# Optimization experiments

Measured on AMD Instinct MI355X. Metric: run time of the kernel, lower is better.

The kernel has to match this reference:

```python
import jax, jax.numpy as jnp
import numpy as np
from jax import lax

B_, NCH, T = 128, 22, 1000
F1, F2 = 8, 16
BN_EPS = 1e-5


def _conv(x, w, b, pad, groups=1):
    y = lax.conv_general_dilated(x, w, (1, 1), pad,
                                 dimension_numbers=('NCHW', 'OIHW', 'NCHW'),
                                 feature_group_count=groups)
    return y if b is None else y + b[None, :, None, None]


def _bn(x, g, b):
    # eval-mode BatchNorm2d with running_mean=0, running_var=1
    return x * (g / np.sqrt(1.0 + BN_EPS))[None, :, None, None] + b[None, :, None, None]


def _avgpool(x, w, s):
    y = lax.reduce_window(x, 0.0, lax.add, (1, 1, 1, w), (1, 1, 1, s), 'VALID')
    return y / w


def _ln(x, g, b):
    m = x.mean(-1, keepdims=True)
    v = ((x - m) ** 2).mean(-1, keepdims=True)
    return (x - m) * lax.rsqrt(v + 1e-5) * g + b


def _enc_layer(h, qw, qb, pw, pb, f1w, f1b, f2w, f2b, g1, b1, g2, b2):
    # h: (S, N, E). Torch TransformerEncoderLayer default is seq-first, so axis 0
    # (the STDCNN batch dim) is attended over -- faithfully reproduced here.
    S, N, E = h.shape
    H = 8
    hd = E // H
    q, k, v = jnp.split(h @ qw.T + qb, 3, axis=-1)
    q = q.reshape(S, N, H, hd)
    k = k.reshape(S, N, H, hd)
    v = v.reshape(S, N, H, hd)
    att = jax.nn.softmax(jnp.einsum('snhd,tnhd->nhst', q, k) / np.sqrt(hd), axis=-1)
    o = jnp.einsum('nhst,tnhd->snhd', att, v).reshape(S, N, E) @ pw.T + pb
    h = _ln(h + o, g1, b1)
    ff = jax.nn.relu(h @ f1w.T + f1b) @ f2w.T + f2b
    return _ln(h + ff, g2, b2)


def setup_inputs() -> dict:
    key = jax.random.key(0)
    ks = iter(jax.random.split(key, 48))

    def nrm(shape, s=0.1):
        return jax.random.normal(next(ks), shape, jnp.float32) * s

    inp = dict(
        x=jax.random.normal(next(ks), (B_, 1, NCH, T), jnp.float32),
        w_spec1=nrm((F1, 1, 1, 125)), b_spec1=nrm((F1,)),
        w_spec2=nrm((F1, 1, 1, 30)), b_spec2=nrm((F1,)),
        g_bn1=1.0 + nrm((F1,)), b_bn1=nrm((F1,)),
        g_bn2=1.0 + nrm((F1,)), b_bn2=nrm((F1,)),
        w_sp1a=nrm((F2, 1, NCH, 1)),
        g_bn3=1.0 + nrm((F2,)), b_bn3=nrm((F2,)),
        w_sp1b=nrm((F2, F2, 1, 1)), b_sp1b=nrm((F2,)),
        g_bn4=1.0 + nrm((F2,)), b_bn4=nrm((F2,)),
        w_sp2=nrm((F2, F1, NCH, 1)), b_sp2=nrm((F2,)),
        g_bn5=1.0 + nrm((F2,)), b_bn5=nrm((F2,)),
        A=jnp.eye(F2, dtype=jnp.float32) + nrm((F2, F2), 0.01),
        Bm=nrm((F2, F2)),
        Cm=jnp.eye(F2, dtype=jnp.float32) + nrm((F2, F2), 0.01),
        qkv_w=nrm((2, 3 * F2, F2)), qkv_b=nrm((2, 3 * F2)),
        proj_w=nrm((2, F2, F2)), proj_b=nrm((2, F2)),
        ff1_w=nrm((2, 64, F2)), ff1_b=nrm((2, 64)),
        ff2_w=nrm((2, F2, 64)), ff2_b=nrm((2, F2)),
        ln1_g=jnp.ones((2, F2), jnp.float32), ln1_b=jnp.zeros((2, F2), jnp.float32),
        ln2_g=jnp.ones((2, F2), jnp.float32), ln2_b=jnp.zeros((2, F2), jnp.float32),
    )
    return inp


def reference(x, w_spec1, b_spec1, w_spec2, b_spec2, g_bn1, b_bn1, g_bn2, b_bn2,
              w_sp1a, g_bn3, b_bn3, w_sp1b, b_sp1b, g_bn4, b_bn4,
              w_sp2, b_sp2, g_bn5, b_bn5, A, Bm, Cm,
              qkv_w, qkv_b, proj_w, proj_b, ff1_w, ff1_b, ff2_w, ff2_b,
              ln1_g, ln1_b, ln2_g, ln2_b):
    # spectral branches (torch 'same' padding: k=125 -> (62,62); k=30 -> (14,15))
    x1 = _bn(_conv(x, w_spec1, b_spec1, [(0, 0), (62, 62)]), g_bn1, b_bn1)
    x2 = _bn(_conv(x, w_spec2, b_spec2, [(0, 0), (14, 15)]), g_bn2, b_bn2)
    # spatial branch 1 (dropout is identity in eval)
    s1 = jax.nn.elu(_bn(_conv(x1, w_sp1a, None, 'VALID', groups=F1), g_bn3, b_bn3))
    s1 = jax.nn.elu(_bn(_conv(s1, w_sp1b, b_sp1b, 'VALID'), g_bn4, b_bn4))
    s1 = _avgpool(s1, 32, 32)                                   # (B,16,1,31)
    # spatial branch 2: square -> avgpool -> log(clamp)
    s2 = _bn(_conv(x2, w_sp2, b_sp2, 'VALID'), g_bn5, b_bn5)
    s2 = jnp.log(jnp.clip(_avgpool(jnp.square(s2), 75, 25), 1e-6))  # (B,16,1,38)
    xc = jnp.concatenate([s1, s2], axis=3)                       # (B,16,1,69)
    Bn, Cc, H2, W2 = xc.shape
    seq = xc.reshape(Bn, Cc, H2 * W2).transpose(0, 2, 1)         # (B,L,16)

    # linear SSM recurrence (torch for-loop -> lax.scan)
    def step(state, xt):
        state = state @ A + xt @ Bm.T
        return state, state @ Cm.T

    _, outs = lax.scan(step, jnp.zeros((Bn, F2), seq.dtype), seq.transpose(1, 0, 2))
    h = outs.transpose(1, 0, 2)                                  # (B,L,16)

    for l in range(2):
        h = _enc_layer(h, qkv_w[l], qkv_b[l], proj_w[l], proj_b[l],
                       ff1_w[l], ff1_b[l], ff2_w[l], ff2_b[l],
                       ln1_g[l], ln1_b[l], ln2_g[l], ln2_b[l])

    return h.reshape(Bn, W2, 1, Cc).transpose(0, 3, 2, 1)        # (B,16,1,69)
```

## Files before the change

kernel.cpp:

```cpp
#include <hip/hip_runtime.h>
#include <hip/hip_bf16.h>
#include <math.h>

#define BBATCH 128
#define NCHAN  22
#define TLEN   1000
#define F1C    8
#define F2C    16
#define L1W    31
#define L2W    38
#define LSEQ   69
#define EDIM   16
#define NHEAD  8
#define FFDIM  64

#define C_SA   0
#define C_BA   16
#define C_BC2  32
#define C_AW   4144
#define C_AW1  (C_AW + 5632)
#define C_TOTAL (C_AW1 + 22528)

#define OFF_CONST 0
#define OFF_CHNK  40960
#define OFF_SEQ   (OFF_CHNK + 81920)
#define OFF_STB   (OFF_SEQ + 141312)
#define OFF_HBUF  (OFF_STB + 141312)

typedef __attribute__((ext_vector_type(8))) short bf16x8;
typedef __attribute__((ext_vector_type(4))) float f32x4;

static __device__ __forceinline__ unsigned short f2bf(float f) {
    unsigned u = __float_as_uint(f);
    unsigned r = (u + 0x7FFFu + ((u >> 16) & 1u)) >> 16;
    return (unsigned short)r;
}

#define SWZ(v, imm) __int_as_float(__builtin_amdgcn_ds_swizzle(__float_as_int(v), imm))
#define MV16(dst, sv, W) do { \
    float p0=SWZ(sv,0x010)*W[0],  p1=SWZ(sv,0x030)*W[1],  \
          p2=SWZ(sv,0x050)*W[2],  p3=SWZ(sv,0x070)*W[3],  \
          p4=SWZ(sv,0x090)*W[4],  p5=SWZ(sv,0x0B0)*W[5],  \
          p6=SWZ(sv,0x0D0)*W[6],  p7=SWZ(sv,0x0F0)*W[7],  \
          p8=SWZ(sv,0x110)*W[8],  p9=SWZ(sv,0x130)*W[9],  \
          p10=SWZ(sv,0x150)*W[10],p11=SWZ(sv,0x170)*W[11],\
          p12=SWZ(sv,0x190)*W[12],p13=SWZ(sv,0x1B0)*W[13],\
          p14=SWZ(sv,0x1D0)*W[14],p15=SWZ(sv,0x1F0)*W[15];\
    dst = (((p0+p1)+(p2+p3))+((p4+p5)+(p6+p7))) + (((p8+p9)+(p10+p11))+((p12+p13)+(p14+p15))); \
} while(0)

__global__ void k_setup(const float* __restrict__ wsp1a, const float* __restrict__ b_spec1,
                        const float* __restrict__ g_bn1, const float* __restrict__ b_bn1,
                        const float* __restrict__ g_bn3, const float* __restrict__ b_bn3,
                        const float* __restrict__ w_spec2, const float* __restrict__ b_spec2,
                        const float* __restrict__ g_bn2, const float* __restrict__ b_bn2,
                        const float* __restrict__ w_sp2, const float* __restrict__ b_sp2,
                        const float* __restrict__ g_bn5, const float* __restrict__ b_bn5,
                        const float* __restrict__ w_spec1,
                        float* __restrict__ consts)
{
    int tid = threadIdx.x;
    int gb = blockIdx.x;
    int NG = gridDim.x;
    int gid = gb*256 + tid;
    float rbn = rsqrtf(1.0f + 1e-5f);
    if (gb == 0 && tid < 16) {
        int c2 = tid, c1 = c2 >> 1;
        float wsum = 0.f;
        for (int h = 0; h < NCHAN; h++) wsum += wsp1a[c2*NCHAN + h];
        float s1b = g_bn1[c1] * rbn;
        float s3  = g_bn3[c2] * rbn;
        float C1  = (s1b * b_spec1[c1] + b_bn1[c1]) * wsum;
        consts[C_SA + c2] = s3 * s1b;
        consts[C_BA + c2] = s3 * C1 + b_bn3[c2];
        float s5 = g_bn5[c2] * rbn;
        float acc = b_sp2[c2];
        for (int cc = 0; cc < F1C; cc++) {
            float s2b = g_bn2[cc] * rbn;
            float cb  = s2b * b_spec2[cc] + b_bn2[cc];
            float wsh = 0.f;
            for (int h = 0; h < NCHAN; h++) wsh += w_sp2[(c2*F1C + cc)*NCHAN + h];
            acc += wsh * cb;
        }
        consts[C_BC2 + c2] = s5 * acc + b_bn5[c2];
    }
    unsigned* aw = (unsigned*)&consts[C_AW];
    for (int idx = gid; idx < 22*64*4; idx += 256*NG) {
        int r = idx & 3;
        int l = (idx >> 2) & 63;
        int c = idx >> 8;
        int m = l & 15;
        int k0 = ((l >> 4) << 3) + 2*r;
        float s5 = g_bn5[m] * rbn;
        float w0 = 0.f, w1 = 0.f;
        for (int cc = 0; cc < F1C; cc++) {
            float f = w_sp2[(m*F1C + cc)*NCHAN + c] * (g_bn2[cc] * rbn);
            if (k0 < 30)     w0 += f * w_spec2[cc*30 + k0];
            if (k0 + 1 < 30) w1 += f * w_spec2[cc*30 + k0 + 1];
        }
        w0 *= s5; w1 *= s5;
        aw[idx] = (unsigned)f2bf(w0) | ((unsigned)f2bf(w1) << 16);
    }
    unsigned* aw1 = (unsigned*)&consts[C_AW1];
    for (int idx = gid; idx < 22*4*64*4; idx += 256*NG) {
        int r = idx & 3;
        int l = (idx >> 2) & 63;
        int kk = (idx >> 8) & 3;
        int c = idx >> 10;
        int m = l & 15;
        int klocal = ((l >> 4) << 3) + 2*r;
        int tap0 = kk*32 + klocal;
        float sa = (g_bn3[m] * rbn) * (g_bn1[m >> 1] * rbn);
        float base = sa * wsp1a[m*NCHAN + c];
        float w0 = (tap0     < 125) ? base * w_spec1[(m >> 1)*125 + tap0]     : 0.f;
        float w1 = (tap0 + 1 < 125) ? base * w_spec1[(m >> 1)*125 + tap0 + 1] : 0.f;
        aw1[idx] = (unsigned)f2bf(w0) | ((unsigned)f2bf(w1) << 16);
    }
}

#define PB1 384
#define NW1 (NCHAN*PB1)
#define PS1 257
#define PB2 288
#define SQP2 257
#define FRONT_SM 12560

__device__ __forceinline__ void b1mm_body(float* smem, int bid,
    const float* __restrict__ x, const float* __restrict__ consts,
    const float* __restrict__ w_sp1b, const float* __restrict__ b_sp1b,
    const float* __restrict__ g_bn4, const float* __restrict__ b_bn4,
    float* __restrict__ seq)
{
    unsigned short* xs = (unsigned short*)smem;
    float* sq = smem + 8448;
    const uint4* __restrict__ awg = (const uint4*)&consts[C_AW1];
    int q = bid & 3, b = bid >> 2;
    int t0 = q * 256;
    int tid = threadIdx.x;

    for (int idx = tid; idx < NW1; idx += 256) {
        int h = idx / PB1, e = idx - h*PB1;
        int t = t0 - 62 + e;
        const float* xr = x + (b*NCHAN + h)*TLEN;
        float v0 = ((unsigned)t < 1000u && e < 380) ? xr[t] : 0.f;
        float v1 = ((unsigned)(t+1) < 1000u && e < 380) ? xr[t+1] : 0.f;
        xs[idx] = f2bf(v0);
        xs[NW1 + idx] = f2bf(v1);
    }
    __syncthreads();

    int lane = tid & 63, wid = tid >> 6;
    int tp = lane & 15;
    int kb = (lane >> 4) << 3;
    int P = tp & 1;
    int tb0 = wid * 64;
    const unsigned short* xb = xs + P*NW1 + (tb0 + tp + kb - P);

    f32x4 a0 = {0.f,0.f,0.f,0.f};
    f32x4 a1 = a0, a2 = a0, a3 = a0;
    for (int c = 0; c < NCHAN; c++) {
#pragma unroll
        for (int kk = 0; kk < 4; kk++) {
            uint4 au = awg[(c*4 + kk)*64 + lane];
            union Ua { uint4 qv; bf16x8 v; } A; A.qv = au;
            const unsigned short* row = xb + c*PB1 + kk*32;
            union Uv { bf16x8 v; unsigned u[4]; };
            Uv B0, B1, B2, B3;
#pragma unroll
            for (int r = 0; r < 4; r++) {
                B0.u[r] = *(const unsigned*)(row + 2*r);
                B1.u[r] = *(const unsigned*)(row + 16 + 2*r);
                B2.u[r] = *(const unsigned*)(row + 32 + 2*r);
                B3.u[r] = *(const unsigned*)(row + 48 + 2*r);
            }
            a0 = __builtin_amdgcn_mfma_f32_16x16x32_bf16(A.v, B0.v, a0, 0, 0, 0);
            a1 = __builtin_amdgcn_mfma_f32_16x16x32_bf16(A.v, B1.v, a1, 0, 0, 0);
            a2 = __builtin_amdgcn_mfma_f32_16x16x32_bf16(A.v, B2.v, a2, 0, 0, 0);
            a3 = __builtin_amdgcn_mfma_f32_16x16x32_bf16(A.v, B3.v, a3, 0, 0, 0);
        }
    }

    {
        int c2b = (lane >> 4) * 4;
        float ba[4];
#pragma unroll
        for (int r = 0; r < 4; r++) ba[r] = consts[C_BA + c2b + r];
#pragma unroll
        for (int r = 0; r < 4; r++) {
            float v, e;
            v = a0[r] + ba[r]; e = (v > 0.f) ? v : (expf(v) - 1.f);
            sq[(c2b+r)*PS1 + tb0 + tp +  0] = e;
            v = a1[r] + ba[r]; e = (v > 0.f) ? v : (expf(v) - 1.f);
            sq[(c2b+r)*PS1 + tb0 + tp + 16] = e;
            v = a2[r] + ba[r]; e = (v > 0.f) ? v : (expf(v) - 1.f);
            sq[(c2b+r)*PS1 + tb0 + tp + 32] = e;
            v = a3[r] + ba[r]; e = (v > 0.f) ? v : (expf(v) - 1.f);
            sq[(c2b+r)*PS1 + tb0 + tp + 48] = e;
        }
    }
    __syncthreads();

    {
        int u = tid;
        int w = 8*q + (u >> 5);
        float rbn = rsqrtf(1.0f + 1e-5f);
        float hv[16];
#pragma unroll
        for (int c = 0; c < 16; c++) hv[c] = sq[c*PS1 + u];
        float p[16];
#pragma unroll
        for (int c = 0; c < 16; c++) {
            float s = 0.f;
#pragma unroll
            for (int j = 0; j < 16; j++) s += w_sp1b[c*16 + j] * hv[j];
            float sc = g_bn4[c] * rbn;
            float a = sc * (s + b_sp1b[c]) + b_bn4[c];
            float g = (a > 0.f) ? a : (expf(a) - 1.f);
            g += __shfl_xor(g, 1, 64);
            g += __shfl_xor(g, 2, 64);
            g += __shfl_xor(g, 4, 64);
            g += __shfl_xor(g, 8, 64);
            g += __shfl_xor(g, 16, 64);
            p[c] = g;
        }
        if ((u & 31) == 0 && w < L1W) {
            float* sp = &seq[(b*LSEQ + w)*16];
#pragma unroll
            for (int i = 0; i < 4; i++)
                *(float4*)&sp[4*i] = make_float4(p[4*i]*(1.f/32.f), p[4*i+1]*(1.f/32.f),
                                                 p[4*i+2]*(1.f/32.f), p[4*i+3]*(1.f/32.f));
        }
    }
}

__device__ __forceinline__ void b2mm_body(float* smem, int bid,
    const float* __restrict__ x, const float* __restrict__ consts,
    float* __restrict__ chnk)
{
    unsigned short* xs = (unsigned short*)smem;
    float* sq = smem + 6336;
    const unsigned* __restrict__ awg = (const unsigned*)&consts[C_AW];
    int q = bid & 3, b = bid >> 2;
    int t0 = q * 250;
    int tid = threadIdx.x;

    for (int idx = tid; idx < NCHAN*PB2; idx += 256) {
        int h = idx / PB2, e = idx - h*PB2;
        int t = t0 - 14 + e;
        const float* xr = x + (b*NCHAN + h)*TLEN;
        float v0 = ((unsigned)t < 1000u) ? xr[t] : 0.f;
        float v1 = ((unsigned)(t+1) < 1000u) ? xr[t+1] : 0.f;
        xs[idx] = f2bf(v0);
        xs[NCHAN*PB2 + idx] = f2bf(v1);
    }
    __syncthreads();

    int lane = tid & 63, wid = tid >> 6;
    int tp = lane & 15;
    int kb = (lane >> 4) << 3;
    int P = tp & 1;
    int tb0 = wid * 64;
    const unsigned short* xb = xs + P*(NCHAN*PB2) + (tb0 + tp + kb - P);

    f32x4 a0 = {0.f,0.f,0.f,0.f};
    f32x4 a1 = a0, a2 = a0, a3 = a0;
    for (int c = 0; c < NCHAN; c++) {
        bf16x8 af = *(const bf16x8*)(awg + (c*64 + lane)*4);
        const unsigned short* row = xb + c*PB2;
        union Uv { bf16x8 v; unsigned u[4]; };
        Uv B0, B1, B2, B3;
#pragma unroll
        for (int r = 0; r < 4; r++) {
            B0.u[r] = *(const unsigned*)(row + 2*r);
            B1.u[r] = *(const unsigned*)(row + 16 + 2*r);
            B2.u[r] = *(const unsigned*)(row + 32 + 2*r);
            B3.u[r] = *(const unsigned*)(row + 48 + 2*r);
        }
        a0 = __builtin_amdgcn_mfma_f32_16x16x32_bf16(af, B0.v, a0, 0, 0, 0);
        a1 = __builtin_amdgcn_mfma_f32_16x16x32_bf16(af, B1.v, a1, 0, 0, 0);
        a2 = __builtin_amdgcn_mfma_f32_16x16x32_bf16(af, B2.v, a2, 0, 0, 0);
        a3 = __builtin_amdgcn_mfma_f32_16x16x32_bf16(af, B3.v, a3, 0, 0, 0);
    }

    {
        int c2b = (lane >> 4) * 4;
        float bc[4];
#pragma unroll
        for (int r = 0; r < 4; r++) bc[r] = consts[C_BC2 + c2b + r];
#pragma unroll
        for (int r = 0; r < 4; r++) {
            float v;
            v = a0[r] + bc[r]; sq[(c2b+r)*SQP2 + tb0 + tp +  0] = v*v;
            v = a1[r] + bc[r]; sq[(c2b+r)*SQP2 + tb0 + tp + 16] = v*v;
            v = a2[r] + bc[r]; sq[(c2b+r)*SQP2 + tb0 + tp + 32] = v*v;
            v = a3[r] + bc[r]; sq[(c2b+r)*SQP2 + tb0 + tp + 48] = v*v;
        }
    }
    __syncthreads();

    if (tid < 160) {
        int c2 = tid / 10, ch = tid % 10;
        const float* s = &sq[c2*SQP2 + ch*25];
        float acc2 = 0.f;
#pragma unroll
        for (int i = 0; i < 25; i++) acc2 += s[i];
        chnk[(b*16 + c2)*40 + q*10 + ch] = acc2;
    }
}

__global__ __launch_bounds__(256, 2)
void k_front(const float* __restrict__ x,
             const float* __restrict__ consts,
             const float* __restrict__ w_sp1b, const float* __restrict__ b_sp1b,
             const float* __restrict__ g_bn4, const float* __restrict__ b_bn4,
             float* __restrict__ seq, float* __restrict__ chnk)
{
    __shared__ __align__(16) float smem[FRONT_SM];
    int bid = blockIdx.x;
    if (bid < BBATCH*4) {
        b1mm_body(smem, bid, x, consts, w_sp1b, b_sp1b, g_bn4, b_bn4, seq);
    } else {
        b2mm_body(smem, bid - BBATCH*4, x, consts, chnk);
    }
}

__global__ __launch_bounds__(64, 1)
void k_ssm(const float* __restrict__ seq, const float* __restrict__ chnk,
           const float* __restrict__ Amat, const float* __restrict__ Bmat,
           float* __restrict__ stbuf)
{
    int tid = threadIdx.x;
    int j = tid & 15;
    int b = blockIdx.x * 4 + (tid >> 4);

    float Acol[16], Brow[16];
#pragma unroll
    for (int i = 0; i < 16; i++) {
        Acol[i] = Amat[i*16 + j];
        Brow[i] = Bmat[j*16 + i];
    }

    float xv[LSEQ];
#pragma unroll
    for (int l = 0; l < 31; l++) xv[l] = seq[(b*LSEQ + l)*16 + j];
    {
        float cp[40];
        const float4* cpp = (const float4*)(chnk + (b*16 + j)*40);
#pragma unroll
        for (int i = 0; i < 10; i++) {
            float4 v = cpp[i];
            cp[4*i]=v.x; cp[4*i+1]=v.y; cp[4*i+2]=v.z; cp[4*i+3]=v.w;
        }
#pragma unroll
        for (int w = 0; w < 38; w++) {
            float m = (cp[w] + cp[w+1] + cp[w+2]) * (1.f/75.f);
            xv[31 + w] = logf(fmaxf(m, 1e-6f));
        }
    }

#pragma unroll
    for (int l = 0; l < LSEQ; l++) {
        float u;
        MV16(u, xv[l], Brow);
        xv[l] = u;
    }

    float st = 0.f;
#pragma unroll
    for (int l = 0; l < LSEQ; l++) {
        float nv;
        MV16(nv, st, Acol);
        st = nv + xv[l];
        stbuf[(l*BBATCH + b)*16 + j] = st;
    }
}

#define KVS2 38
#define F1S 17
__global__ __launch_bounds__(256, 2)
void k_tfl(const float* __restrict__ hin, const float* __restrict__ Cmat, int applyC,
           const float* __restrict__ qw, const float* __restrict__ qb,
           const float* __restrict__ pw, const float* __restrict__ pb,
           const float* __restrict__ f1w, const float* __restrict__ f1b,
           const float* __restrict__ f2w, const float* __restrict__ f2b,
           const float* __restrict__ g1, const float* __restrict__ b1,
           const float* __restrict__ g2, const float* __restrict__ b2,
           float* __restrict__ hout, float* __restrict__ fout, int writeFinal)
{
    __shared__ __align__(16) float sm[2176 + 128*KVS2 + 576 + 544 + 7*544 + 64*F1S + 1024 + 64];
    float* h_l  = sm;
    float* kvq  = sm + 2176;
    float* qbuf = sm + 2176 + 128*KVS2;
    float* olds = qbuf + 576;
    float* ffp  = olds + 544;
    float* f1l  = ffp + 7*544;
    float* f2l  = f1l + 64*F1S;
    float* f1bl = f2l + 1024;

    int tid = threadIdx.x;
    int rl = tid >> 3, hh = tid & 7;
    int n = blockIdx.x >> 2, q2 = blockIdx.x & 3;
    int s = q2*32 + rl;

    for (int i = tid; i < 1024; i += 256) {
        f1l[(i >> 4)*F1S + (i & 15)] = f1w[i];
        f2l[i] = f2w[i];
    }
    if (tid < 64) f1bl[tid] = f1b[tid];

    {
        int r = tid >> 1, qd = tid & 1;
        if (applyC) {
            const float4* fr = (const float4*)(hin + (n*BBATCH + r)*16);
            float rv[16];
#pragma unroll
            for (int i = 0; i < 4; i++) {
                float4 a = fr[i];
                rv[4*i]=a.x; rv[4*i+1]=a.y; rv[4*i+2]=a.z; rv[4*i+3]=a.w;
            }
#pragma unroll
            for (int cq = 0; cq < 8; cq++) {
                int c = 8*qd + cq;
                float sum = 0.f;
#pragma unroll
                for (int i = 0; i < 16; i++) sum += rv[i] * Cmat[c*16 + i];
                h_l[r*17 + c] = sum;
            }
        } else {
            const float4* sr = (const float4*)(hin + (n*BBATCH + r)*16 + qd*8);
            float4 a0 = sr[0];
            float4 a1 = sr[1];
            h_l[r*17 + qd*8 + 0] = a0.x; h_l[r*17 + qd*8 + 1] = a0.y;
            h_l[r*17 + qd*8 + 2] = a0.z; h_l[r*17 + qd*8 + 3] = a0.w;
            h_l[r*17 + qd*8 + 4] = a1.x; h_l[r*17 + qd*8 + 5] = a1.y;
            h_l[r*17 + qd*8 + 6] = a1.z; h_l[r*17 + qd*8 + 7] = a1.w;
        }
    }
    __syncthreads();

    {
        int r2 = tid & 127;
        int ob = 16 + (tid >> 7) * 16;
        float hv[16];
#pragma unroll
        for (int c = 0; c < 16; c++) hv[c] = h_l[r2*17 + c];
#pragma unroll
        for (int oq = 0; oq < 16; oq++) {
            int o = ob + oq;
            float sum = qb[o];
#pragma unroll
            for (int c = 0; c < 16; c++) sum += qw[o*16 + c] * hv[c];
            kvq[r2*KVS2 + (o - 16)] = sum;
        }
        if (tid < 32) {
            int sr = q2*32 + tid;
            float hq[16];
#pragma unroll
            for (int c = 0; c < 16; c++) hq[c] = h_l[sr*17 + c];
#pragma unroll
            for (int o = 0; o < 16; o++) {
                float sum = qb[o];
#pragma unroll
                for (int c = 0; c < 16; c++) sum += qw[o*16 + c] * hq[c];
                qbuf[tid*18 + o] = sum;
            }
        }
    }
    __syncthreads();

    {
        const float SC = 1.0201941311775597f;
        float q0 = qbuf[rl*18 + 2*hh] * SC;
        float q1 = qbuf[rl*18 + 2*hh + 1] * SC;
        const float* kbase = &kvq[2*hh];
        float m0 = -1e30f, m1 = -1e30f, m2 = -1e30f, m3 = -1e30f;
#pragma unroll
        for (int tb = 0; tb < 128; tb += 4) {
            float2 k0 = *(const float2*)&kbase[(tb+0)*KVS2];
            float2 k1 = *(const float2*)&kbase[(tb+1)*KVS2];
            float2 k2 = *(const float2*)&kbase[(tb+2)*KVS2];
            float2 k3 = *(const float2*)&kbase[(tb+3)*KVS2];
            m0 = fmaxf(m0, q0*k0.x + q1*k0.y);
            m1 = fmaxf(m1, q0*k1.x + q1*k1.y);
            m2 = fmaxf(m2, q0*k2.x + q1*k2.y);
            m3 = fmaxf(m3, q0*k3.x + q1*k3.y);
        }
        float M = fmaxf(fmaxf(m0, m1), fmaxf(m2, m3));
        float su0 = 0.f, su1 = 0.f, su2 = 0.f, su3 = 0.f;
        float av0 = 0.f, av1 = 0.f, av2 = 0.f, av3 = 0.f;
        float bv0 = 0.f, bv1 = 0.f, bv2 = 0.f, bv3 = 0.f;
#pragma unroll
        for (int tb = 0; tb < 128; tb += 4) {
            float2 k0 = *(const float2*)&kbase[(tb+0)*KVS2];
            float2 k1 = *(const float2*)&kbase[(tb+1)*KVS2];
            float2 k2 = *(const float2*)&kbase[(tb+2)*KVS2];
            float2 k3 = *(const float2*)&kbase[(tb+3)*KVS2];
            float2 v0 = *(const float2*)&kbase[(tb+0)*KVS2 + 16];
            float2 v1 = *(const float2*)&kbase[(tb+1)*KVS2 + 16];
            float2 v2 = *(const float2*)&kbase[(tb+2)*KVS2 + 16];
            float2 v3 = *(const float2*)&kbase[(tb+3)*KVS2 + 16];
            float e0 = exp2f(q0*k0.x + q1*k0.y - M);
            float e1 = exp2f(q0*k1.x + q1*k1.y - M);
            float e2 = exp2f(q0*k2.x + q1*k2.y - M);
            float e3 = exp2f(q0*k3.x + q1*k3.y - M);
            su0 += e0; av0 += e0*v0.x; bv0 += e0*v0.y;
            su1 += e1; av1 += e1*v1.x; bv1 += e1*v1.y;
            su2 += e2; av2 += e2*v2.x; bv2 += e2*v2.y;
            su3 += e3; av3 += e3*v3.x; bv3 += e3*v3.y;
        }
        float su = (su0 + su1) + (su2 + su3);
        float av = (av0 + av1) + (av2 + av3);
        float bv = (bv0 + bv1) + (bv2 + bv3);
        float inv = 1.f / su;
        olds[rl*17 + 2*hh + 0] = av * inv;
        olds[rl*17 + 2*hh + 1] = bv * inv;
    }
    __syncthreads();

    {
        float rv[16], ov[16];
#pragma unroll
        for (int c = 0; c < 16; c++) { rv[c] = h_l[s*17 + c]; ov[c] = olds[rl*17 + c]; }
        float h1[16];
#pragma unroll
        for (int c = 0; c < 16; c++) {
            float p = pb[c];
#pragma unroll
            for (int j = 0; j < 16; j++) p += pw[c*16 + j] * ov[j];
            h1[c] = rv[c] + p;
        }
        float mn = 0.f;
#pragma unroll
        for (int c = 0; c < 16; c++) mn += h1[c];
        mn *= (1.f/16.f);
        float var = 0.f;
#pragma unroll
        for (int c = 0; c < 16; c++) { float d = h1[c] - mn; var += d*d; }
        var *= (1.f/16.f);
        float rs = rsqrtf(var + 1e-5f);
        float y[16];
#pragma unroll
        for (int c = 0; c < 16; c++) y[c] = (h1[c] - mn)*rs*g1[c] + b1[c];

        float t2[16];
#pragma unroll
        for (int c = 0; c < 16; c++) t2[c] = (hh == 0) ? f2b[c] : 0.f;
#pragma unroll
        for (int uq = 0; uq < 8; uq++) {
            int u = 8*hh + uq;
            float sv = f1bl[u];
#pragma unroll
            for (int c = 0; c < 16; c++) sv += f1l[u*F1S + c] * y[c];
            sv = fmaxf(sv, 0.f);
#pragma unroll
            for (int c = 0; c < 16; c++) t2[c] += f2l[c*64 + u] * sv;
        }
        if (hh) {
#pragma unroll
            for (int c = 0; c < 16; c++) ffp[(hh-1)*544 + rl*17 + c] = t2[c];
        }
        __syncthreads();
        if (hh == 0) {
#pragma unroll
            for (int k = 0; k < 7; k++)
#pragma unroll
                for (int c = 0; c < 16; c++) t2[c] += ffp[k*544 + rl*17 + c];
            float h2[16];
#pragma unroll
            for (int c = 0; c < 16; c++) h2[c] = y[c] + t2[c];
            mn = 0.f;
#pragma unroll
            for (int c = 0; c < 16; c++) mn += h2[c];
            mn *= (1.f/16.f);
            var = 0.f;
#pragma unroll
            for (int c = 0; c < 16; c++) { float d = h2[c] - mn; var += d*d; }
            var *= (1.f/16.f);
            rs = rsqrtf(var + 1e-5f);
            if (writeFinal) {
#pragma unroll
                for (int c = 0; c < 16; c++)
                    fout[(s*16 + c)*LSEQ + n] = (h2[c] - mn)*rs*g2[c] + b2[c];
            } else {
                float z[16];
#pragma unroll
                for (int c = 0; c < 16; c++) z[c] = (h2[c] - mn)*rs*g2[c] + b2[c];
                float* hp = hout + (n*BBATCH + s)*16;
#pragma unroll
                for (int i = 0; i < 4; i++)
                    *(float4*)&hp[4*i] = make_float4(z[4*i], z[4*i+1], z[4*i+2], z[4*i+3]);
            }
        }
    }
}

extern "C" void kernel_launch(void* const* d_in, const int* in_sizes, int n_in,
                              void* d_out, int out_size, void* d_ws, size_t ws_size,
                              hipStream_t stream)
{
    const float* x       = (const float*)d_in[0];
    const float* w_spec1 = (const float*)d_in[1];
    const float* b_spec1 = (const float*)d_in[2];
    const float* w_spec2 = (const float*)d_in[3];
    const float* b_spec2 = (const float*)d_in[4];
    const float* g_bn1   = (const float*)d_in[5];
    const float* b_bn1   = (const float*)d_in[6];
    const float* g_bn2   = (const float*)d_in[7];
    const float* b_bn2   = (const float*)d_in[8];
    const float* w_sp1a  = (const float*)d_in[9];
    const float* g_bn3   = (const float*)d_in[10];
    const float* b_bn3   = (const float*)d_in[11];
    const float* w_sp1b  = (const float*)d_in[12];
    const float* b_sp1b  = (const float*)d_in[13];
    const float* g_bn4   = (const float*)d_in[14];
    const float* b_bn4   = (const float*)d_in[15];
    const float* w_sp2   = (const float*)d_in[16];
    const float* b_sp2   = (const float*)d_in[17];
    const float* g_bn5   = (const float*)d_in[18];
    const float* b_bn5   = (const float*)d_in[19];
    const float* Amat    = (const float*)d_in[20];
    const float* Bmat    = (const float*)d_in[21];
    const float* Cmat    = (const float*)d_in[22];
    const float* qkv_w   = (const float*)d_in[23];
    const float* qkv_b   = (const float*)d_in[24];
    const float* proj_w  = (const float*)d_in[25];
    const float* proj_b  = (const float*)d_in[26];
    const float* ff1_w   = (const float*)d_in[27];
    const float* ff1_b   = (const float*)d_in[28];
    const float* ff2_w   = (const float*)d_in[29];
    const float* ff2_b   = (const float*)d_in[30];
    const float* ln1_g   = (const float*)d_in[31];
    const float* ln1_b   = (const float*)d_in[32];
    const float* ln2_g   = (const float*)d_in[33];
    const float* ln2_b   = (const float*)d_in[34];

    float* ws  = (float*)d_ws;
    float* out = (float*)d_out;

    float* consts = ws + OFF_CONST;
    float* chnk   = ws + OFF_CHNK;
    float* seq    = ws + OFF_SEQ;
    float* stbuf  = ws + OFF_STB;
    float* hbuf   = ws + OFF_HBUF;

    k_setup<<<24, 256, 0, stream>>>(w_sp1a, b_spec1, g_bn1, b_bn1, g_bn3, b_bn3,
                                    w_spec2, b_spec2, g_bn2, b_bn2,
                                    w_sp2, b_sp2, g_bn5, b_bn5, w_spec1, consts);
    k_front<<<BBATCH*4 + BBATCH*4, 256, 0, stream>>>(x, consts,
        w_sp1b, b_sp1b, g_bn4, b_bn4, seq, chnk);
    k_ssm<<<BBATCH/4, 64, 0, stream>>>(seq, chnk, Amat, Bmat, stbuf);

    k_tfl<<<LSEQ*4, 256, 0, stream>>>(stbuf, Cmat, 1,
        qkv_w, qkv_b, proj_w, proj_b, ff1_w, ff1_b, ff2_w, ff2_b,
        ln1_g, ln1_b, ln2_g, ln2_b, hbuf, out, 0);
    k_tfl<<<LSEQ*4, 256, 0, stream>>>(hbuf, Cmat, 0,
        qkv_w + 768, qkv_b + 48, proj_w + 256, proj_b + 16,
        ff1_w + 1024, ff1_b + 64, ff2_w + 1024, ff2_b + 16,
        ln1_g + 16, ln1_b + 16, ln2_g + 16, ln2_b + 16, hbuf, out, 1);
}
```

Baseline: 116.9 us.

## Pad front-end shared buffers, raise occupancy, stage transformer weights in LDS

Offsets the second (odd-shifted) bf16 copy of the input tile in shared memory by 16 elements in both front-end branches, intended to shift LDS bank mapping between the two parity copies. It raises the front kernel's launch_bounds minimum blocks per CU from 2 to 3, which caps register use per thread. In the transformer-layer kernel, the C matrix, QKV weights and biases, projection weights and LayerNorm parameters are copied into shared memory once per block instead of being read from global memory inside unrolled loops. The costs are slightly more LDS per block, an extra barrier, and possible register spills under the tighter launch bound.

Result: slower. 150.5 us (+28.8%).

```diff
diff --git a/kernel.cpp b/kernel.cpp
--- a/kernel.cpp
+++ b/kernel.cpp
@@ -120,10 +120,13 @@
 
 #define PB1 384
 #define NW1 (NCHAN*PB1)
+#define CP1 (NW1 + 16)
 #define PS1 257
 #define PB2 288
+#define NW2 (NCHAN*PB2)
+#define CP2 (NW2 + 16)
 #define SQP2 257
-#define FRONT_SM 12560
+#define FRONT_SM 12568
 
 __device__ __forceinline__ void b1mm_body(float* smem, int bid,
     const float* __restrict__ x, const float* __restrict__ consts,
@@ -132,7 +135,7 @@
     float* __restrict__ seq)
 {
     unsigned short* xs = (unsigned short*)smem;
-    float* sq = smem + 8448;
+    float* sq = smem + 8456;
     const uint4* __restrict__ awg = (const uint4*)&consts[C_AW1];
     int q = bid & 3, b = bid >> 2;
     int t0 = q * 256;
@@ -145,7 +148,7 @@
         float v0 = ((unsigned)t < 1000u && e < 380) ? xr[t] : 0.f;
         float v1 = ((unsigned)(t+1) < 1000u && e < 380) ? xr[t+1] : 0.f;
         xs[idx] = f2bf(v0);
-        xs[NW1 + idx] = f2bf(v1);
+        xs[CP1 + idx] = f2bf(v1);
     }
     __syncthreads();
 
@@ -154,7 +157,7 @@
     int kb = (lane >> 4) << 3;
     int P = tp & 1;
     int tb0 = wid * 64;
-    const unsigned short* xb = xs + P*NW1 + (tb0 + tp + kb - P);
+    const unsigned short* xb = xs + P*CP1 + (tb0 + tp + kb - P);
 
     f32x4 a0 = {0.f,0.f,0.f,0.f};
     f32x4 a1 = a0, a2 = a0, a3 = a0;
@@ -238,20 +241,20 @@
     float* __restrict__ chnk)
 {
     unsigned short* xs = (unsigned short*)smem;
-    float* sq = smem + 6336;
+    float* sq = smem + 6344;
     const unsigned* __restrict__ awg = (const unsigned*)&consts[C_AW];
     int q = bid & 3, b = bid >> 2;
     int t0 = q * 250;
     int tid = threadIdx.x;
 
-    for (int idx = tid; idx < NCHAN*PB2; idx += 256) {
+    for (int idx = tid; idx < NW2; idx += 256) {
         int h = idx / PB2, e = idx - h*PB2;
         int t = t0 - 14 + e;
         const float* xr = x + (b*NCHAN + h)*TLEN;
         float v0 = ((unsigned)t < 1000u) ? xr[t] : 0.f;
         float v1 = ((unsigned)(t+1) < 1000u) ? xr[t+1] : 0.f;
         xs[idx] = f2bf(v0);
-        xs[NCHAN*PB2 + idx] = f2bf(v1);
+        xs[CP2 + idx] = f2bf(v1);
     }
     __syncthreads();
 
@@ -260,7 +263,7 @@
     int kb = (lane >> 4) << 3;
     int P = tp & 1;
     int tb0 = wid * 64;
-    const unsigned short* xb = xs + P*(NCHAN*PB2) + (tb0 + tp + kb - P);
+    const unsigned short* xb = xs + P*CP2 + (tb0 + tp + kb - P);
 
     f32x4 a0 = {0.f,0.f,0.f,0.f};
     f32x4 a1 = a0, a2 = a0, a3 = a0;
@@ -308,7 +311,7 @@
     }
 }
 
-__global__ __launch_bounds__(256, 2)
+__global__ __launch_bounds__(256, 3)
 void k_front(const float* __restrict__ x,
              const float* __restrict__ consts,
              const float* __restrict__ w_sp1b, const float* __restrict__ b_sp1b,
@@ -387,7 +390,9 @@
            const float* __restrict__ g2, const float* __restrict__ b2,
            float* __restrict__ hout, float* __restrict__ fout, int writeFinal)
 {
-    __shared__ __align__(16) float sm[2176 + 128*KVS2 + 576 + 544 + 7*544 + 64*F1S + 1024 + 64];
+    __shared__ __align__(16) float sm[2176 + 128*KVS2 + 576 + 544 + 7*544
+                                      + 64*F1S + 1024 + 64
+                                      + 256 + 768 + 48 + 256 + 16 + 64];
     float* h_l  = sm;
     float* kvq  = sm + 2176;
     float* qbuf = sm + 2176 + 128*KVS2;
@@ -396,6 +401,12 @@
     float* f1l  = ffp + 7*544;
     float* f2l  = f1l + 64*F1S;
     float* f1bl = f2l + 1024;
+    float* cml  = f1bl + 64;
+    float* qwl  = cml + 256;
+    float* qbl  = qwl + 768;
+    float* pwl  = qbl + 48;
+    float* pbl  = pwl + 256;
+    float* lnl  = pbl + 16;
 
     int tid = threadIdx.x;
     int rl = tid >> 3, hh = tid & 7;
@@ -406,7 +417,16 @@
         f1l[(i >> 4)*F1S + (i & 15)] = f1w[i];
         f2l[i] = f2w[i];
     }
+    for (int i = tid; i < 768; i += 256) qwl[i] = qw[i];
+    if (tid < 256) { cml[tid] = Cmat[tid]; pwl[tid] = pw[tid]; }
     if (tid < 64) f1bl[tid] = f1b[tid];
+    if (tid < 48) qbl[tid] = qb[tid];
+    if (tid < 16) {
+        pbl[tid] = pb[tid];
+        lnl[tid] = g1[tid]; lnl[16 + tid] = b1[tid];
+        lnl[32 + tid] = g2[tid]; lnl[48 + tid] = b2[tid];
+    }
+    __syncthreads();
 
     {
         int r = tid >> 1, qd = tid & 1;
@@ -423,7 +443,7 @@
                 int c = 8*qd + cq;
                 float sum = 0.f;
 #pragma unroll
-                for (int i = 0; i < 16; i++) sum += rv[i] * Cmat[c*16 + i];
+                for (int i = 0; i < 16; i++) sum += rv[i] * cml[c*16 + i];
                 h_l[r*17 + c] = sum;
             }
         } else {
@@ -447,9 +467,9 @@
 #pragma unroll
         for (int oq = 0; oq < 16; oq++) {
             int o = ob + oq;
-            float sum = qb[o];
-#pragma unroll
-            for (int c = 0; c < 16; c++) sum += qw[o*16 + c] * hv[c];
+            float sum = qbl[o];
+#pragma unroll
+            for (int c = 0; c < 16; c++) sum += qwl[o*16 + c] * hv[c];
             kvq[r2*KVS2 + (o - 16)] = sum;
         }
         if (tid < 32) {
@@ -459,9 +479,9 @@
             for (int c = 0; c < 16; c++) hq[c] = h_l[sr*17 + c];
 #pragma unroll
             for (int o = 0; o < 16; o++) {
-                float sum = qb[o];
-#pragma unroll
-                for (int c = 0; c < 16; c++) sum += qw[o*16 + c] * hq[c];
+                float sum = qbl[o];
+#pragma unroll
+                for (int c = 0; c < 16; c++) sum += qwl[o*16 + c] * hq[c];
                 qbuf[tid*18 + o] = sum;
             }
         }
@@ -524,9 +544,9 @@
         float h1[16];
 #pragma unroll
         for (int c = 0; c < 16; c++) {
-            float p = pb[c];
-#pragma unroll
-            for (int j = 0; j < 16; j++) p += pw[c*16 + j] * ov[j];
+            float p = pbl[c];
+#pragma unroll
+            for (int j = 0; j < 16; j++) p += pwl[c*16 + j] * ov[j];
             h1[c] = rv[c] + p;
         }
         float mn = 0.f;
@@ -540,7 +560,7 @@
         float rs = rsqrtf(var + 1e-5f);
         float y[16];
 #pragma unroll
-        for (int c = 0; c < 16; c++) y[c] = (h1[c] - mn)*rs*g1[c] + b1[c];
+        for (int c = 0; c < 16; c++) y[c] = (h1[c] - mn)*rs*lnl[c] + lnl[16 + c];
 
         float t2[16];
 #pragma unroll
@@ -580,11 +600,11 @@
             if (writeFinal) {
 #pragma unroll
                 for (int c = 0; c < 16; c++)
-                    fout[(s*16 + c)*LSEQ + n] = (h2[c] - mn)*rs*g2[c] + b2[c];
+                    fout[(s*16 + c)*LSEQ + n] = (h2[c] - mn)*rs*lnl[32 + c] + lnl[48 + c];
             } else {
                 float z[16];
 #pragma unroll
-                for (int c = 0; c < 16; c++) z[c] = (h2[c] - mn)*rs*g2[c] + b2[c];
+                for (int c = 0; c < 16; c++) z[c] = (h2[c] - mn)*rs*lnl[32 + c] + lnl[48 + c];
                 float* hp = hout + (n*BBATCH + s)*16;
 #pragma unroll
                 for (int i = 0; i < 4; i++)
```
